# Optimization experiments

Measured on AMD Instinct MI355X. Metric: run time of the kernel, lower is better.

The kernel has to match this reference:

```python
import jax, jax.numpy as jnp
import numpy as np

HEADS = 8
DIM_HEAD = 64
EPS = 1e-4
SCALE = DIM_HEAD ** -0.5


def setup_inputs() -> dict:
    key = jax.random.key(0)
    k1, k2, k3, k4 = jax.random.split(key, 4)
    dim = HEADS * DIM_HEAD  # 512
    x = jax.random.normal(k1, (2, 2048, dim), dtype=jnp.float32)
    # torch Linear weights are [out, in]; scale like default init
    Wq = jax.random.normal(k2, (dim, dim), dtype=jnp.float32) / np.sqrt(dim)
    Wkv = jax.random.normal(k3, (2 * dim, dim), dtype=jnp.float32) / np.sqrt(dim)
    Wout = jax.random.normal(k4, (dim, dim), dtype=jnp.float32) / np.sqrt(dim)
    return {"x": x, "Wq": Wq, "Wkv": Wkv, "Wout": Wout}


def _normalize_magnitude(t, eps=EPS):
    # divide by (sqrt(mean(t^2, -1)) + eps)
    mag = jnp.sqrt(jnp.mean(t * t, axis=-1, keepdims=True)) + eps
    return t / mag


def reference(x, Wq, Wkv, Wout):
    b, n, dim = x.shape
    h, d = HEADS, DIM_HEAD
    # norm=False -> Identity; context = x (self-attention)
    q = x @ Wq.T                      # [b, n, h*d]
    kv = x @ Wkv.T                    # [b, n, 2*h*d]
    k, v = jnp.split(kv, 2, axis=-1)
    def to_heads(t):
        return t.reshape(b, n, h, d).transpose(0, 2, 1, 3)  # [b, h, n, d]
    q, k, v = map(to_heads, (q, k, v))
    q = _normalize_magnitude(q)
    k = _normalize_magnitude(k)
    sim = jnp.einsum('bhid,bhjd->bhij', q, k) * SCALE
    attn = jax.nn.softmax(sim, axis=-1)
    out = jnp.einsum('bhij,bhjd->bhid', attn, v)
    out = out.transpose(0, 2, 1, 3).reshape(b, n, h * d)
    return out @ Wout.T
```

## Files before the change

### kernel.cpp

```cpp
#include <hip/hip_runtime.h>

typedef __bf16 bf16x8 __attribute__((ext_vector_type(8)));
typedef __bf16 bf16x4 __attribute__((ext_vector_type(4)));
typedef float  f32x4  __attribute__((ext_vector_type(4)));

#define LOG2E_F 1.44269504088896340736f

static constexpr int kB = 2, kN = 2048, kH = 8, kD = 64, kDim = 512;
static constexpr int kTok = kB * kN;
static constexpr int kNQKV = 1536;

__device__ __forceinline__ void gld16(const void* g, void* l) {
  __builtin_amdgcn_global_load_lds(
      (const __attribute__((address_space(1))) void*)g,
      (__attribute__((address_space(3))) void*)l, 16, 0, 0);
}

__global__ __launch_bounds__(256) void cvt_all(const float* __restrict__ x,
                                               const float* __restrict__ wq,
                                               const float* __restrict__ wkv,
                                               const float* __restrict__ wo,
                                               __bf16* __restrict__ xb,
                                               __bf16* __restrict__ wqkvb,
                                               __bf16* __restrict__ wob) {
  size_t i = ((size_t)blockIdx.x * 256 + threadIdx.x) * 8;
  const float* s; __bf16* d; size_t off;
  if (i < 2097152)      { s = x;   d = xb;              off = i; }
  else if (i < 2359296) { s = wq;  d = wqkvb;           off = i - 2097152; }
  else if (i < 2883584) { s = wkv; d = wqkvb + 262144;  off = i - 2359296; }
  else                  { s = wo;  d = wob;             off = i - 2883584; }
  float4 u = *(const float4*)(s + off);
  float4 v = *(const float4*)(s + off + 4);
  bf16x8 t;
  t[0] = (__bf16)u.x; t[1] = (__bf16)u.y; t[2] = (__bf16)u.z; t[3] = (__bf16)u.w;
  t[4] = (__bf16)v.x; t[5] = (__bf16)v.y; t[6] = (__bf16)v.z; t[7] = (__bf16)v.w;
  *(bf16x8*)(d + off) = t;
}

__global__ __launch_bounds__(256, 3) void gemm_qkv(const __bf16* __restrict__ A,
                                                   const __bf16* __restrict__ B,
                                                   __bf16* __restrict__ qn,
                                                   __bf16* __restrict__ kn,
                                                   __bf16* __restrict__ vt2) {
  const int K = kDim;
  const int tid = threadIdx.x;
  const int w = tid >> 6, lane = tid & 63, quad = lane >> 4, lq = lane & 15;
  const int m0 = blockIdx.y * 128;
  const int n0 = blockIdx.x * 64;
  const int wm = w * 32;
  __shared__ __bf16 As[2][128 * 64];
  __shared__ __bf16 Bs[2][64 * 64];

  const f32x4 zero = {0.f, 0.f, 0.f, 0.f};
  f32x4 acc[2][4];
#pragma unroll
  for (int fm = 0; fm < 2; ++fm)
#pragma unroll
    for (int fn = 0; fn < 4; ++fn) acc[fm][fn] = zero;

  const int sr = tid >> 3, sc = (tid & 7) << 3;
  auto stage = [&](int k0, int buf) {
#pragma unroll
    for (int j = 0; j < 4; ++j)
      gld16(A + (size_t)(m0 + j * 32 + sr) * K + k0 + sc,
            &As[buf][(size_t)(j * 32 + sr) * 64 + sc]);
#pragma unroll
    for (int j = 0; j < 2; ++j)
      gld16(B + (size_t)(n0 + j * 32 + sr) * K + k0 + sc,
            &Bs[buf][(size_t)(j * 32 + sr) * 64 + sc]);
  };

  stage(0, 0);
  for (int i = 0; i < 8; ++i) {
    __syncthreads();
    if (i + 1 < 8) stage((i + 1) << 6, (i + 1) & 1);
    const __bf16* as = As[i & 1];
    const __bf16* bs = Bs[i & 1];
#pragma unroll
    for (int ks = 0; ks < 2; ++ks) {
      bf16x8 a[2], b[4];
#pragma unroll
      for (int fm = 0; fm < 2; ++fm)
        a[fm] = *(const bf16x8*)&as[(wm + fm * 16 + lq) * 64 + ks * 32 + quad * 8];
#pragma unroll
      for (int fn = 0; fn < 4; ++fn)
        b[fn] = *(const bf16x8*)&bs[(fn * 16 + lq) * 64 + ks * 32 + quad * 8];
#pragma unroll
      for (int fm = 0; fm < 2; ++fm)
#pragma unroll
        for (int fn = 0; fn < 4; ++fn)
          acc[fm][fn] =
              __builtin_amdgcn_mfma_f32_16x16x32_bf16(a[fm], b[fn], acc[fm][fn], 0, 0, 0);
    }
  }

  const int h = (n0 >> 6) & 7;
  if (n0 >= 1024) {
#pragma unroll
    for (int fm = 0; fm < 2; ++fm)
#pragma unroll
      for (int r = 0; r < 4; ++r) {
        const int m = m0 + wm + fm * 16 + quad * 4 + r;
        const int b = m >> 11, n = m & (kN - 1);
        const int kt = n >> 6, tt = n & 63;
        const int p = (tt & 15) * 4 + (tt >> 4);
        const size_t base = (size_t)(((b * kH + h) * 32 + kt) * 64) * 64 + p;
#pragma unroll
        for (int fn = 0; fn < 4; ++fn)
          vt2[base + (size_t)(fn * 16 + lq) * 64] = (__bf16)acc[fm][fn][r];
      }
  } else {
    const float qs = (n0 < 512) ? (0.125f * LOG2E_F) : 1.0f;
    __bf16* dst0 = (n0 < 512) ? qn : kn;
#pragma unroll
    for (int fm = 0; fm < 2; ++fm)
#pragma unroll
      for (int r = 0; r < 4; ++r) {
        float ss = 0.f;
#pragma unroll
        for (int fn = 0; fn < 4; ++fn) ss += acc[fm][fn][r] * acc[fm][fn][r];
#pragma unroll
        for (int off = 1; off < 16; off <<= 1) ss += __shfl_xor(ss, off, 64);
        const float inv = qs / (sqrtf(ss * (1.f / 64)) + 1e-4f);
        const int m = m0 + wm + fm * 16 + quad * 4 + r;
        const int b = m >> 11, n = m & (kN - 1);
        __bf16* dst = dst0 + ((size_t)(b * kH + h) * kN + n) * kD;
#pragma unroll
        for (int fn = 0; fn < 4; ++fn)
          dst[fn * 16 + lq] = (__bf16)(acc[fm][fn][r] * inv);
      }
  }
}

__global__ __launch_bounds__(256, 2) void attn(const __bf16* __restrict__ qn,
                                               const __bf16* __restrict__ kn,
                                               const __bf16* __restrict__ vt2,
                                               __bf16* __restrict__ po,
                                               float* __restrict__ pl) {
  const int qt = blockIdx.x, bh = blockIdx.y, kh = blockIdx.z;
  const int tid = threadIdx.x;
  const int w = tid >> 6, lane = tid & 63, quad = lane >> 4, lq = lane & 15;
  __shared__ __bf16 Ks[2][4096];
  __shared__ __bf16 Vs[2][4096];
  __shared__ __bf16 Ps[4][32 * 72];
  __bf16* myP = Ps[w];

  bf16x8 aq[2][2];
#pragma unroll
  for (int fm = 0; fm < 2; ++fm) {
    const __bf16* Qb = qn + ((size_t)bh * kN + qt * 128 + w * 32 + fm * 16 + lq) * kD;
    aq[fm][0] = *(const bf16x8*)(Qb + quad * 8);
    aq[fm][1] = *(const bf16x8*)(Qb + 32 + quad * 8);
  }

  const f32x4 zero  = {0.f, 0.f, 0.f, 0.f};
  const f32x4 minit = {-12.f, -12.f, -12.f, -12.f};
  f32x4 o[2][4];
  float lr[2][4];
#pragma unroll
  for (int fm = 0; fm < 2; ++fm)
#pragma unroll
    for (int i = 0; i < 4; ++i) { o[fm][i] = zero; lr[fm][i] = 0.f; }

  const __bf16* Kb = kn + ((size_t)bh * kN + kh * 1024) * kD;
  const __bf16* Vb = vt2 + (size_t)(bh * 32 + kh * 16) * 4096;

  auto stage = [&](int kt, int buf) {
#pragma unroll
    for (int j = 0; j < 2; ++j) {
      gld16(Kb + (size_t)kt * 4096 + (j * 256 + tid) * 8, &Ks[buf][(j * 256 + tid) * 8]);
      gld16(Vb + (size_t)kt * 4096 + (j * 256 + tid) * 8, &Vs[buf][(j * 256 + tid) * 8]);
    }
  };

  stage(0, 0);
#pragma unroll 2
  for (int kt = 0; kt < 16; ++kt) {
    __syncthreads();
    if (kt < 15) stage(kt + 1, (kt + 1) & 1);
    const __bf16* ks_ = Ks[kt & 1];
    const __bf16* vs_ = Vs[kt & 1];

    bf16x8 kb0[4], kb1[4], vb0[4], vb1[4];
#pragma unroll
    for (int fn = 0; fn < 4; ++fn) {
      const int row = fn * 16 + lq;
      kb0[fn] = *(const bf16x8*)&ks_[row * 64 + quad * 8];
      kb1[fn] = *(const bf16x8*)&ks_[row * 64 + 32 + quad * 8];
      vb0[fn] = *(const bf16x8*)&vs_[row * 64 + quad * 8];
      vb1[fn] = *(const bf16x8*)&vs_[row * 64 + 32 + quad * 8];
    }
    f32x4 s[2][4];
#pragma unroll
    for (int fm = 0; fm < 2; ++fm)
#pragma unroll
      for (int fn = 0; fn < 4; ++fn) {
        f32x4 a = __builtin_amdgcn_mfma_f32_16x16x32_bf16(aq[fm][0], kb0[fn], minit, 0, 0, 0);
        s[fm][fn] = __builtin_amdgcn_mfma_f32_16x16x32_bf16(aq[fm][1], kb1[fn], a, 0, 0, 0);
      }

#pragma unroll
    for (int fm = 0; fm < 2; ++fm)
#pragma unroll
      for (int r = 0; r < 4; ++r) {
        const float p0 = __builtin_amdgcn_exp2f(s[fm][0][r]);
        const float p1 = __builtin_amdgcn_exp2f(s[fm][1][r]);
        const float p2 = __builtin_amdgcn_exp2f(s[fm][2][r]);
        const float p3 = __builtin_amdgcn_exp2f(s[fm][3][r]);
        lr[fm][r] += (p0 + p1) + (p2 + p3);
        bf16x4 pk = {(__bf16)p0, (__bf16)p1, (__bf16)p2, (__bf16)p3};
        *(bf16x4*)&myP[(fm * 16 + quad * 4 + r) * 72 + lq * 4] = pk;
      }

#pragma unroll
    for (int fm = 0; fm < 2; ++fm) {
      bf16x8 ap0 = *(const bf16x8*)&myP[(fm * 16 + lq) * 72 + quad * 8];
      bf16x8 ap1 = *(const bf16x8*)&myP[(fm * 16 + lq) * 72 + 32 + quad * 8];
#pragma unroll
      for (int fn = 0; fn < 4; ++fn) {
        o[fm][fn] = __builtin_amdgcn_mfma_f32_16x16x32_bf16(ap0, vb0[fn], o[fm][fn], 0, 0, 0);
        o[fm][fn] = __builtin_amdgcn_mfma_f32_16x16x32_bf16(ap1, vb1[fn], o[fm][fn], 0, 0, 0);
      }
    }
  }

  const int b = bh >> 3, h = bh & 7;
#pragma unroll
  for (int fm = 0; fm < 2; ++fm) {
    const int qrow0 = qt * 128 + w * 32 + fm * 16 + quad * 4;
#pragma unroll
    for (int r = 0; r < 4; ++r) {
      float sum = lr[fm][r];
#pragma unroll
      for (int off = 1; off < 16; off <<= 1) sum += __shfl_xor(sum, off, 64);
      if (lq == 0) pl[(size_t)kh * 32768 + bh * kN + qrow0 + r] = sum;
      const size_t ob = ((size_t)kh * kTok + b * kN + qrow0 + r) * kDim + h * 64;
#pragma unroll
      for (int fn = 0; fn < 4; ++fn) po[ob + fn * 16 + lq] = (__bf16)o[fm][fn][r];
    }
  }
}

__global__ __launch_bounds__(256) void combine(const __bf16* __restrict__ po,
                                               const float* __restrict__ pl,
                                               __bf16* __restrict__ ao) {
  const size_t i = ((size_t)blockIdx.x * 256 + threadIdx.x) * 4;
  const int tok = (int)(i >> 9), dk = (int)(i & 511);
  const int h = dk >> 6, b = tok >> 11, qrow = tok & (kN - 1);
  const int bh = b * kH + h;
  const float l = pl[bh * kN + qrow] + pl[32768 + bh * kN + qrow];
  const float inv = 1.f / l;
  bf16x4 a = *(const bf16x4*)(po + i);
  bf16x4 c = *(const bf16x4*)(po + (size_t)kTok * kDim + i);
  bf16x4 t = {(__bf16)(((float)a[0] + (float)c[0]) * inv),
              (__bf16)(((float)a[1] + (float)c[1]) * inv),
              (__bf16)(((float)a[2] + (float)c[2]) * inv),
              (__bf16)(((float)a[3] + (float)c[3]) * inv)};
  *(bf16x4*)(ao + i) = t;
}

__global__ __launch_bounds__(256, 3) void gemm128(const __bf16* __restrict__ A,
                                                  const __bf16* __restrict__ B,
                                                  float* __restrict__ C,
                                                  int N, int K) {
  const int tid = threadIdx.x;
  const int w = tid >> 6, lane = tid & 63, quad = lane >> 4, lq = lane & 15;
  const int m0 = blockIdx.y * 128;
  const int n0 = blockIdx.x * 64;
  const int wm = w * 32;
  __shared__ __bf16 As[2][128 * 64];
  __shared__ __bf16 Bs[2][64 * 64];

  const f32x4 zero = {0.f, 0.f, 0.f, 0.f};
  f32x4 acc[2][4];
#pragma unroll
  for (int fm = 0; fm < 2; ++fm)
#pragma unroll
    for (int fn = 0; fn < 4; ++fn) acc[fm][fn] = zero;

  const int sr = tid >> 3, sc = (tid & 7) << 3;
  auto stage = [&](int k0, int buf) {
#pragma unroll
    for (int j = 0; j < 4; ++j)
      gld16(A + (size_t)(m0 + j * 32 + sr) * K + k0 + sc,
            &As[buf][(size_t)(j * 32 + sr) * 64 + sc]);
#pragma unroll
    for (int j = 0; j < 2; ++j)
      gld16(B + (size_t)(n0 + j * 32 + sr) * K + k0 + sc,
            &Bs[buf][(size_t)(j * 32 + sr) * 64 + sc]);
  };

  stage(0, 0);
  const int iters = K >> 6;
  for (int i = 0; i < iters; ++i) {
    __syncthreads();
    if (i + 1 < iters) stage((i + 1) << 6, (i + 1) & 1);
    const __bf16* as = As[i & 1];
    const __bf16* bs = Bs[i & 1];
#pragma unroll
    for (int ks = 0; ks < 2; ++ks) {
      bf16x8 a[2], b[4];
#pragma unroll
      for (int fm = 0; fm < 2; ++fm)
        a[fm] = *(const bf16x8*)&as[(wm + fm * 16 + lq) * 64 + ks * 32 + quad * 8];
#pragma unroll
      for (int fn = 0; fn < 4; ++fn)
        b[fn] = *(const bf16x8*)&bs[(fn * 16 + lq) * 64 + ks * 32 + quad * 8];
#pragma unroll
      for (int fm = 0; fm < 2; ++fm)
#pragma unroll
        for (int fn = 0; fn < 4; ++fn)
          acc[fm][fn] =
              __builtin_amdgcn_mfma_f32_16x16x32_bf16(a[fm], b[fn], acc[fm][fn], 0, 0, 0);
    }
  }
#pragma unroll
  for (int fm = 0; fm < 2; ++fm)
#pragma unroll
    for (int fn = 0; fn < 4; ++fn)
#pragma unroll
      for (int r = 0; r < 4; ++r)
        C[(size_t)(m0 + wm + fm * 16 + quad * 4 + r) * N + n0 + fn * 16 + lq] =
            acc[fm][fn][r];
}

extern "C" void kernel_launch(void* const* d_in, const int* in_sizes, int n_in,
                              void* d_out, int out_size, void* d_ws, size_t ws_size,
                              hipStream_t stream) {
  const float* x    = (const float*)d_in[0];
  const float* Wq   = (const float*)d_in[1];
  const float* Wkv  = (const float*)d_in[2];
  const float* Wout = (const float*)d_in[3];
  float* out = (float*)d_out;
  char* ws = (char*)d_ws;

  __bf16* xb    = (__bf16*)(ws);
  __bf16* wqkvb = (__bf16*)(ws + (size_t)(4 << 20));
  __bf16* wob   = (__bf16*)(ws + (size_t)(6 << 20));
  __bf16* qn    = (__bf16*)(ws + (size_t)(7 << 20));
  __bf16* kn    = (__bf16*)(ws + (size_t)(11 << 20));
  __bf16* vt2   = (__bf16*)(ws + (size_t)(15 << 20));
  __bf16* po    = (__bf16*)(ws + (size_t)(19 << 20));
  float*  pl    = (float*)(ws + (size_t)(27 << 20));
  __bf16* ao    = (__bf16*)(ws + (size_t)(28 << 20));

  cvt_all<<<1536, 256, 0, stream>>>(x, Wq, Wkv, Wout, xb, wqkvb, wob);
  gemm_qkv<<<dim3(kNQKV / 64, kTok / 128), 256, 0, stream>>>(xb, wqkvb, qn, kn, vt2);
  attn<<<dim3(kN / 128, kB * kH, 2), 256, 0, stream>>>(qn, kn, vt2, po, pl);
  combine<<<kTok * kDim / 1024, 256, 0, stream>>>(po, pl, ao);
  gemm128<<<dim3(kDim / 64, kTok / 128), 256, 0, stream>>>(ao, wob, out, kDim, kDim);
}
```

Before: 130.4 us.

## Split attention keys four ways, stage V-transpose through LDS, shrink output GEMM tiles

Attention now splits the key sequence into four chunks instead of two, giving four times more blocks per head, and combine sums four partial outputs and denominators. The QKV GEMM epilogue for V writes the transposed tile into LDS first and then issues coalesced 16-byte global stores instead of scattered 2-byte stores. The output GEMM uses 64x64 tiles with a 2x2 wave layout to double the grid size. The aim is more parallelism on the many CUs and cheaper V writes, at the cost of more partial-result traffic in combine and less reuse per GEMM tile.

Result: no change. 129.7 us (-0.5%).

```diff
diff --git a/kernel.cpp b/kernel.cpp
--- a/kernel.cpp
+++ b/kernel.cpp
@@ -9,6 +9,7 @@
 static constexpr int kB = 2, kN = 2048, kH = 8, kD = 64, kDim = 512;
 static constexpr int kTok = kB * kN;
 static constexpr int kNQKV = 1536;
+static constexpr int kKH = 4;
 
 __device__ __forceinline__ void gld16(const void* g, void* l) {
   __builtin_amdgcn_global_load_lds(
@@ -96,19 +97,29 @@
 
   const int h = (n0 >> 6) & 7;
   if (n0 >= 1024) {
+    __syncthreads();
+    __bf16* Ts = &As[0][0];
 #pragma unroll
     for (int fm = 0; fm < 2; ++fm)
 #pragma unroll
       for (int r = 0; r < 4; ++r) {
-        const int m = m0 + wm + fm * 16 + quad * 4 + r;
-        const int b = m >> 11, n = m & (kN - 1);
-        const int kt = n >> 6, tt = n & 63;
+        const int mo = wm + fm * 16 + quad * 4 + r;
+        const int tau = mo >> 6, tt = mo & 63;
         const int p = (tt & 15) * 4 + (tt >> 4);
-        const size_t base = (size_t)(((b * kH + h) * 32 + kt) * 64) * 64 + p;
 #pragma unroll
         for (int fn = 0; fn < 4; ++fn)
-          vt2[base + (size_t)(fn * 16 + lq) * 64] = (__bf16)acc[fm][fn][r];
-      }
+          Ts[tau * 4608 + (fn * 16 + lq) * 72 + p] = (__bf16)acc[fm][fn][r];
+      }
+    __syncthreads();
+    const int b = m0 >> 11, kt0 = (m0 & (kN - 1)) >> 6;
+    const int dd = tid >> 2, p0 = (tid & 3) << 4;
+#pragma unroll
+    for (int tau = 0; tau < 2; ++tau) {
+      const __bf16* src = Ts + tau * 4608 + dd * 72 + p0;
+      __bf16* dst = vt2 + ((size_t)((b * kH + h) * 32 + kt0 + tau)) * 4096 + tid * 16;
+      *(bf16x8*)dst = *(const bf16x8*)src;
+      *(bf16x8*)(dst + 8) = *(const bf16x8*)(src + 8);
+    }
   } else {
     const float qs = (n0 < 512) ? (0.125f * LOG2E_F) : 1.0f;
     __bf16* dst0 = (n0 < 512) ? qn : kn;
@@ -162,8 +173,8 @@
 #pragma unroll
     for (int i = 0; i < 4; ++i) { o[fm][i] = zero; lr[fm][i] = 0.f; }
 
-  const __bf16* Kb = kn + ((size_t)bh * kN + kh * 1024) * kD;
-  const __bf16* Vb = vt2 + (size_t)(bh * 32 + kh * 16) * 4096;
+  const __bf16* Kb = kn + ((size_t)bh * kN + kh * 512) * kD;
+  const __bf16* Vb = vt2 + (size_t)(bh * 32 + kh * 8) * 4096;
 
   auto stage = [&](int kt, int buf) {
 #pragma unroll
@@ -175,9 +186,9 @@
 
   stage(0, 0);
 #pragma unroll 2
-  for (int kt = 0; kt < 16; ++kt) {
-    __syncthreads();
-    if (kt < 15) stage(kt + 1, (kt + 1) & 1);
+  for (int kt = 0; kt < 8; ++kt) {
+    __syncthreads();
+    if (kt < 7) stage(kt + 1, (kt + 1) & 1);
     const __bf16* ks_ = Ks[kt & 1];
     const __bf16* vs_ = Vs[kt & 1];
 
@@ -247,47 +258,46 @@
   const size_t i = ((size_t)blockIdx.x * 256 + threadIdx.x) * 4;
   const int tok = (int)(i >> 9), dk = (int)(i & 511);
   const int h = dk >> 6, b = tok >> 11, qrow = tok & (kN - 1);
-  const int bh = b * kH + h;
-  const float l = pl[bh * kN + qrow] + pl[32768 + bh * kN + qrow];
+  const int idx = (b * kH + h) * kN + qrow;
+  float l = 0.f;
+#pragma unroll
+  for (int kh = 0; kh < kKH; ++kh) l += pl[kh * 32768 + idx];
   const float inv = 1.f / l;
-  bf16x4 a = *(const bf16x4*)(po + i);
-  bf16x4 c = *(const bf16x4*)(po + (size_t)kTok * kDim + i);
-  bf16x4 t = {(__bf16)(((float)a[0] + (float)c[0]) * inv),
-              (__bf16)(((float)a[1] + (float)c[1]) * inv),
-              (__bf16)(((float)a[2] + (float)c[2]) * inv),
-              (__bf16)(((float)a[3] + (float)c[3]) * inv)};
+  float s0 = 0.f, s1 = 0.f, s2 = 0.f, s3 = 0.f;
+#pragma unroll
+  for (int kh = 0; kh < kKH; ++kh) {
+    bf16x4 a = *(const bf16x4*)(po + (size_t)kh * kTok * kDim + i);
+    s0 += (float)a[0]; s1 += (float)a[1]; s2 += (float)a[2]; s3 += (float)a[3];
+  }
+  bf16x4 t = {(__bf16)(s0 * inv), (__bf16)(s1 * inv),
+              (__bf16)(s2 * inv), (__bf16)(s3 * inv)};
   *(bf16x4*)(ao + i) = t;
 }
 
-__global__ __launch_bounds__(256, 3) void gemm128(const __bf16* __restrict__ A,
-                                                  const __bf16* __restrict__ B,
-                                                  float* __restrict__ C,
-                                                  int N, int K) {
+__global__ __launch_bounds__(256, 2) void gemm64(const __bf16* __restrict__ A,
+                                                 const __bf16* __restrict__ B,
+                                                 float* __restrict__ C,
+                                                 int N, int K) {
   const int tid = threadIdx.x;
   const int w = tid >> 6, lane = tid & 63, quad = lane >> 4, lq = lane & 15;
-  const int m0 = blockIdx.y * 128;
+  const int m0 = blockIdx.y * 64;
   const int n0 = blockIdx.x * 64;
-  const int wm = w * 32;
-  __shared__ __bf16 As[2][128 * 64];
-  __shared__ __bf16 Bs[2][64 * 64];
+  const int wm = (w >> 1) * 32, wn = (w & 1) * 32;
+  __shared__ __bf16 As[2][4096];
+  __shared__ __bf16 Bs[2][4096];
 
   const f32x4 zero = {0.f, 0.f, 0.f, 0.f};
-  f32x4 acc[2][4];
-#pragma unroll
-  for (int fm = 0; fm < 2; ++fm)
-#pragma unroll
-    for (int fn = 0; fn < 4; ++fn) acc[fm][fn] = zero;
+  f32x4 acc00 = zero, acc01 = zero, acc10 = zero, acc11 = zero;
 
   const int sr = tid >> 3, sc = (tid & 7) << 3;
   auto stage = [&](int k0, int buf) {
 #pragma unroll
-    for (int j = 0; j < 4; ++j)
+    for (int j = 0; j < 2; ++j) {
       gld16(A + (size_t)(m0 + j * 32 + sr) * K + k0 + sc,
-            &As[buf][(size_t)(j * 32 + sr) * 64 + sc]);
-#pragma unroll
-    for (int j = 0; j < 2; ++j)
+            &As[buf][(j * 32 + sr) * 64 + sc]);
       gld16(B + (size_t)(n0 + j * 32 + sr) * K + k0 + sc,
-            &Bs[buf][(size_t)(j * 32 + sr) * 64 + sc]);
+            &Bs[buf][(j * 32 + sr) * 64 + sc]);
+    }
   };
 
   stage(0, 0);
@@ -299,29 +309,25 @@
     const __bf16* bs = Bs[i & 1];
 #pragma unroll
     for (int ks = 0; ks < 2; ++ks) {
-      bf16x8 a[2], b[4];
-#pragma unroll
-      for (int fm = 0; fm < 2; ++fm)
-        a[fm] = *(const bf16x8*)&as[(wm + fm * 16 + lq) * 64 + ks * 32 + quad * 8];
-#pragma unroll
-      for (int fn = 0; fn < 4; ++fn)
-        b[fn] = *(const bf16x8*)&bs[(fn * 16 + lq) * 64 + ks * 32 + quad * 8];
-#pragma unroll
-      for (int fm = 0; fm < 2; ++fm)
-#pragma unroll
-        for (int fn = 0; fn < 4; ++fn)
-          acc[fm][fn] =
-              __builtin_amdgcn_mfma_f32_16x16x32_bf16(a[fm], b[fn], acc[fm][fn], 0, 0, 0);
-    }
-  }
+      bf16x8 a0 = *(const bf16x8*)&as[(wm +      lq) * 64 + ks * 32 + quad * 8];
+      bf16x8 a1 = *(const bf16x8*)&as[(wm + 16 + lq) * 64 + ks * 32 + quad * 8];
+      bf16x8 b0 = *(const bf16x8*)&bs[(wn +      lq) * 64 + ks * 32 + quad * 8];
+      bf16x8 b1 = *(const bf16x8*)&bs[(wn + 16 + lq) * 64 + ks * 32 + quad * 8];
+      acc00 = __builtin_amdgcn_mfma_f32_16x16x32_bf16(a0, b0, acc00, 0, 0, 0);
+      acc01 = __builtin_amdgcn_mfma_f32_16x16x32_bf16(a0, b1, acc01, 0, 0, 0);
+      acc10 = __builtin_amdgcn_mfma_f32_16x16x32_bf16(a1, b0, acc10, 0, 0, 0);
+      acc11 = __builtin_amdgcn_mfma_f32_16x16x32_bf16(a1, b1, acc11, 0, 0, 0);
+    }
+  }
+  const f32x4 av[2][2] = {{acc00, acc01}, {acc10, acc11}};
 #pragma unroll
   for (int fm = 0; fm < 2; ++fm)
 #pragma unroll
-    for (int fn = 0; fn < 4; ++fn)
+    for (int fn = 0; fn < 2; ++fn)
 #pragma unroll
       for (int r = 0; r < 4; ++r)
-        C[(size_t)(m0 + wm + fm * 16 + quad * 4 + r) * N + n0 + fn * 16 + lq] =
-            acc[fm][fn][r];
+        C[(size_t)(m0 + wm + fm * 16 + quad * 4 + r) * N + (n0 + wn + fn * 16 + lq)] =
+            av[fm][fn][r];
 }
 
 extern "C" void kernel_launch(void* const* d_in, const int* in_sizes, int n_in,
@@ -341,12 +347,12 @@
   __bf16* kn    = (__bf16*)(ws + (size_t)(11 << 20));
   __bf16* vt2   = (__bf16*)(ws + (size_t)(15 << 20));
   __bf16* po    = (__bf16*)(ws + (size_t)(19 << 20));
-  float*  pl    = (float*)(ws + (size_t)(27 << 20));
-  __bf16* ao    = (__bf16*)(ws + (size_t)(28 << 20));
+  float*  pl    = (float*)(ws + (size_t)(35 << 20));
+  __bf16* ao    = (__bf16*)(ws + (size_t)(36 << 20));
 
   cvt_all<<<1536, 256, 0, stream>>>(x, Wq, Wkv, Wout, xb, wqkvb, wob);
   gemm_qkv<<<dim3(kNQKV / 64, kTok / 128), 256, 0, stream>>>(xb, wqkvb, qn, kn, vt2);
-  attn<<<dim3(kN / 128, kB * kH, 2), 256, 0, stream>>>(qn, kn, vt2, po, pl);
+  attn<<<dim3(kN / 128, kB * kH, kKH), 256, 0, stream>>>(qn, kn, vt2, po, pl);
   combine<<<kTok * kDim / 1024, 256, 0, stream>>>(po, pl, ao);
-  gemm128<<<dim3(kDim / 64, kTok / 128), 256, 0, stream>>>(ao, wob, out, kDim, kDim);
-}
+  gemm64<<<dim3(kDim / 64, kTok / 64), 256, 0, stream>>>(ao, wob, out, kDim, kDim);
+}
```
